# Performance work log

Measured on AMD Instinct MI355X. Metric: run time of the kernel, lower is better.

Reference implementation:

```python
import jax, jax.numpy as jnp
import numpy as np

B = 4096          # events
L = 524288        # total set points (avg 128 per event)
CIN = 16          # per-point feature size (set feature 'a')
DVEC = 32         # flat feature size (feature 'b')
PHI = [128, 128, 64]
MLP = [256, 128]
EPS = 1e-5        # BatchNorm1d eps


def setup_inputs() -> dict:
    key = jax.random.key(0)
    ks = jax.random.split(key, 10)
    def n(k, shape, scale=0.05):
        return jax.random.normal(k, shape, dtype=jnp.float32) * scale
    return {
        "x_a": jax.random.normal(ks[0], (1, CIN, L), dtype=jnp.float32),
        "x_b": jax.random.normal(ks[1], (B, DVEC), dtype=jnp.float32),
        # row 0 -> counts for set feature 'a'; row 1 ignored (Reshape branch)
        "sample_indices": jnp.full((2, B), L // B, dtype=jnp.int32),
        "W1": n(ks[2], (PHI[0], CIN)),  "b1": jnp.zeros((PHI[0],), jnp.float32),
        "W2": n(ks[3], (PHI[1], PHI[0])), "b2": jnp.zeros((PHI[1],), jnp.float32),
        "W3": n(ks[4], (PHI[2], PHI[1])), "b3": jnp.zeros((PHI[2],), jnp.float32),
        "Wm1": n(ks[5], (MLP[0], PHI[2] + DVEC)), "bm1": jnp.zeros((MLP[0],), jnp.float32),
        "g1": jnp.ones((MLP[0],), jnp.float32), "be1": jnp.zeros((MLP[0],), jnp.float32),
        "Wm2": n(ks[6], (MLP[1], MLP[0])), "bm2": jnp.zeros((MLP[1],), jnp.float32),
        "g2": jnp.ones((MLP[1],), jnp.float32), "be2": jnp.zeros((MLP[1],), jnp.float32),
        "Wm3": n(ks[7], (1, MLP[1])), "bm3": jnp.zeros((1,), jnp.float32),
    }


def _bn(x, g, b):
    # BatchNorm1d, training-mode batch stats, biased variance (torch semantics)
    mu = jnp.mean(x, axis=0)
    var = jnp.var(x, axis=0)
    return (x - mu) * jax.lax.rsqrt(var + EPS) * g + b


def reference(x_a, x_b, sample_indices,
              W1, b1, W2, b2, W3, b3,
              Wm1, bm1, g1, be1, Wm2, bm2, g2, be2, Wm3, bm3):
    counts = sample_indices[0].astype(jnp.int32)                       # [B]
    bounds = jnp.concatenate([jnp.zeros((1,), jnp.int32), jnp.cumsum(counts)])  # [B+1]

    # PhiNet: pointwise Conv1d stack (kernel size 1) on [CIN, L]
    h = x_a[0]
    h = jax.nn.relu(jnp.einsum('oc,cl->ol', W1, h) + b1[:, None])
    h = jax.nn.relu(jnp.einsum('oc,cl->ol', W2, h) + b2[:, None])
    h = jax.nn.relu(jnp.einsum('oc,cl->ol', W3, h) + b3[:, None])      # [64, L]

    # fused segment-mean: point p belongs to segment j iff bounds[j] <= p < bounds[j+1]
    seg = jnp.searchsorted(bounds, jnp.arange(h.shape[1], dtype=jnp.int32), side='right') - 1
    sums = jax.ops.segment_sum(h.T, seg, num_segments=counts.shape[0])  # [B, 64]
    means = sums / jnp.maximum(counts, 1).astype(jnp.float32)[:, None]

    # feature order: sorted keys -> ('a' set repr, 'b' flat)
    z = jnp.concatenate([means, x_b.reshape(-1, DVEC)], axis=1)        # [B, 96]

    z = jax.nn.relu(_bn(z @ Wm1.T + bm1, g1, be1))
    z = jax.nn.relu(_bn(z @ Wm2.T + bm2, g2, be2))
    return jax.nn.sigmoid(z @ Wm3.T + bm3)                             # [B, 1]
```

## Files before the change

### kernel.cpp

```cpp
#include <hip/hip_runtime.h>
#include <hip/hip_bf16.h>

#define B_EVENTS 4096
#define L_PTS    524288
#define CIN      16
#define C1       128
#define C2       128
#define C3       64
#define DVEC     32
#define ZDIM     96
#define M1       256
#define M2       128
#define BN_EPS   1e-5f
#define TILE     64
#define NTILES   (L_PTS / TILE)
#define GRID_PHI 2048
#define NTPB     (NTILES / GRID_PHI)

#define XOFF     0
#define H1OFF    4096
#define H2OFF    20480
#define LDSSZ    36864

typedef __attribute__((ext_vector_type(8))) short bf16x8;
typedef __attribute__((ext_vector_type(4))) float f32x4;

__device__ __forceinline__ unsigned cvtpk(float lo, float hi) {
    unsigned r;
    asm("v_cvt_pk_bf16_f32 %0, %1, %2" : "=v"(r) : "v"(lo), "v"(hi));
    return r;
}

__device__ __forceinline__ unsigned long long pack4relub(f32x4 a, f32x4 b) {
    union { unsigned u[2]; unsigned long long ll; } pk;
    pk.u[0] = cvtpk(fmaxf(a[0] + b[0], 0.f), fmaxf(a[1] + b[1], 0.f));
    pk.u[1] = cvtpk(fmaxf(a[2] + b[2], 0.f), fmaxf(a[3] + b[3], 0.f));
    return pk.ll;
}

__device__ __forceinline__ bf16x8 frag_from_f32(const float* p) {
    const float4 lo = *(const float4*)p;
    const float4 hi = *(const float4*)(p + 4);
    union { unsigned u[4]; bf16x8 v; } r;
    r.u[0] = cvtpk(lo.x, lo.y);
    r.u[1] = cvtpk(lo.z, lo.w);
    r.u[2] = cvtpk(hi.x, hi.y);
    r.u[3] = cvtpk(hi.z, hi.w);
    return r.v;
}

__device__ __forceinline__ int ldsoff(int base, int rowSlots, int c, int sir) {
    int s = c * rowSlots + sir;
    s ^= (c & 7);
    return base + s * 16;
}

__device__ __forceinline__ int xaddr(int pt, int g) {
    return XOFF + (((pt * 4 + g) ^ (pt & 7)) * 16);
}

__global__ __launch_bounds__(1024) void scan_kernel(const int* __restrict__ si,
                                                    int* __restrict__ bounds,
                                                    int* __restrict__ tilemap)
{
    __shared__ int sh[1024];
    const int tid = threadIdx.x;
    const int c0 = si[tid*4+0], c1 = si[tid*4+1], c2 = si[tid*4+2], c3 = si[tid*4+3];
    const int s4 = c0 + c1 + c2 + c3;
    sh[tid] = s4;
    __syncthreads();
    for (int off = 1; off < 1024; off <<= 1) {
        int add = (tid >= off) ? sh[tid - off] : 0;
        __syncthreads();
        sh[tid] += add;
        __syncthreads();
    }
    const int excl = (tid == 0) ? 0 : sh[tid - 1];
    bounds[tid*4+0] = excl;
    bounds[tid*4+1] = excl + c0;
    bounds[tid*4+2] = excl + c0 + c1;
    bounds[tid*4+3] = excl + c0 + c1 + c2;
    if (tid == 1023) bounds[B_EVENTS] = excl + s4;
    __syncthreads();

    const int total = bounds[B_EVENTS];
    for (int t = tid; t < NTILES; t += 1024) {
        const int p0 = t * TILE;
        if (p0 >= total) { tilemap[t] = -1; continue; }
        int e = (int)(((long long)p0 * B_EVENTS) / total);
        if (e > B_EVENTS - 1) e = B_EVENTS - 1;
        while (bounds[e] > p0) --e;
        while (bounds[e + 1] <= p0) ++e;
        const bool fast = (p0 + TILE <= bounds[e + 1]);
        tilemap[t] = e | (fast ? (1 << 30) : 0);
    }
}

__global__ __launch_bounds__(256, 3) void phi_mfma_kernel(
    const float* __restrict__ xa,
    const int* __restrict__ bounds, const int* __restrict__ tilemap,
    const float* __restrict__ W1, const float* __restrict__ W2, const float* __restrict__ W3,
    const float* __restrict__ b1, const float* __restrict__ b2, const float* __restrict__ b3,
    float* __restrict__ zsum)
{
    __shared__ __align__(16) char lds[LDSSZ];

    const int tid  = threadIdx.x;
    const int lane = tid & 63;
    const int wm   = tid >> 6;
    const int g4   = lane >> 4;
    const int c16  = lane & 15;

    const int pt = tid & 63;
    const int h  = tid >> 6;
    int t = blockIdx.x;
    float xv[4];
    #pragma unroll
    for (int jj = 0; jj < 4; ++jj)
        xv[jj] = xa[(size_t)(h * 4 + jj) * L_PTS + t * TILE + pt];

    f32x4 bb1[2], bb2[2], bb3;
    #pragma unroll
    for (int mf = 0; mf < 2; ++mf) {
        bb1[mf] = *(const f32x4*)&b1[wm * 32 + mf * 16 + g4 * 4];
        bb2[mf] = *(const f32x4*)&b2[wm * 32 + mf * 16 + g4 * 4];
    }
    bb3 = *(const f32x4*)&b3[wm * 16 + g4 * 4];

    bf16x8 a1[2], a2[2][4], a3[4];
    {
        const bf16x8 zz = {0, 0, 0, 0, 0, 0, 0, 0};
        const int r1 = wm * 32 + c16;
        #pragma unroll
        for (int mf = 0; mf < 2; ++mf)
            a1[mf] = (g4 < 2) ? frag_from_f32(&W1[(r1 + mf * 16) * CIN + g4 * 8]) : zz;
        #pragma unroll
        for (int mf = 0; mf < 2; ++mf)
            #pragma unroll
            for (int kf = 0; kf < 4; ++kf)
                a2[mf][kf] = frag_from_f32(&W2[(r1 + mf * 16) * C1 + kf * 32 + g4 * 8]);
        const int r3 = wm * 16 + c16;
        #pragma unroll
        for (int kf = 0; kf < 4; ++kf)
            a3[kf] = frag_from_f32(&W3[r3 * C2 + kf * 32 + g4 * 8]);
    }

    {
        const int zs = 2 + (h >> 1);
        *(unsigned long long*)(lds + (((pt * 4 + zs) ^ (pt & 7)) * 16) + (h & 1) * 8) = 0ull;
        union { unsigned u[2]; unsigned long long ll; } pk;
        pk.u[0] = cvtpk(xv[0], xv[1]);
        pk.u[1] = cvtpk(xv[2], xv[3]);
        *(unsigned long long*)(lds + xaddr(pt, h >> 1) + (h & 1) * 8) = pk.ll;
    }
    __syncthreads();

    for (int it = 0; it < NTPB; ++it) {
        const int tm = tilemap[t];
        if (tm < 0) break;
        const int  e0    = tm & 0x3FFFFFFF;
        const bool fastp = (tm >> 30) & 1;
        const int  p0    = t * TILE;
        const int  tn    = t + GRID_PHI;
        const bool more  = (it + 1 < NTPB);

        if (more) {
            #pragma unroll
            for (int jj = 0; jj < 4; ++jj)
                xv[jj] = xa[(size_t)(h * 4 + jj) * L_PTS + tn * TILE + pt];
        }

        {
            f32x4 acc[2][4];
            #pragma unroll
            for (int mf = 0; mf < 2; ++mf)
                #pragma unroll
                for (int nf = 0; nf < 4; ++nf)
                    acc[mf][nf] = f32x4{0.f, 0.f, 0.f, 0.f};
            bf16x8 bfr[4];
            #pragma unroll
            for (int nf = 0; nf < 4; ++nf)
                bfr[nf] = *(const bf16x8*)(lds + xaddr(nf * 16 + c16, g4));
            __builtin_amdgcn_s_setprio(1);
            #pragma unroll
            for (int nf = 0; nf < 4; ++nf)
                #pragma unroll
                for (int mf = 0; mf < 2; ++mf)
                    acc[mf][nf] = __builtin_amdgcn_mfma_f32_16x16x32_bf16(a1[mf], bfr[nf], acc[mf][nf], 0, 0, 0);
            __builtin_amdgcn_s_setprio(0);
            #pragma unroll
            for (int mf = 0; mf < 2; ++mf) {
                const int sir = wm * 4 + mf * 2 + (g4 >> 1);
                #pragma unroll
                for (int nf = 0; nf < 4; ++nf) {
                    const int c = nf * 16 + c16;
                    *(unsigned long long*)(lds + ldsoff(H1OFF, 16, c, sir) + (g4 & 1) * 8) = pack4relub(acc[mf][nf], bb1[mf]);
                }
            }
        }
        __syncthreads();

        {
            f32x4 acc[2][4];
            #pragma unroll
            for (int mf = 0; mf < 2; ++mf)
                #pragma unroll
                for (int nf = 0; nf < 4; ++nf)
                    acc[mf][nf] = f32x4{0.f, 0.f, 0.f, 0.f};
            #pragma unroll
            for (int nf = 0; nf < 4; ++nf) {
                const int c = nf * 16 + c16;
                bf16x8 bk[4];
                #pragma unroll
                for (int kf = 0; kf < 4; ++kf)
                    bk[kf] = *(const bf16x8*)(lds + ldsoff(H1OFF, 16, c, kf * 4 + g4));
                __builtin_amdgcn_s_setprio(1);
                #pragma unroll
                for (int mf = 0; mf < 2; ++mf)
                    #pragma unroll
                    for (int kf = 0; kf < 4; ++kf)
                        acc[mf][nf] = __builtin_amdgcn_mfma_f32_16x16x32_bf16(a2[mf][kf], bk[kf], acc[mf][nf], 0, 0, 0);
                __builtin_amdgcn_s_setprio(0);
            }
            if (more) {
                union { unsigned u[2]; unsigned long long ll; } pk;
                pk.u[0] = cvtpk(xv[0], xv[1]);
                pk.u[1] = cvtpk(xv[2], xv[3]);
                *(unsigned long long*)(lds + xaddr(pt, h >> 1) + (h & 1) * 8) = pk.ll;
            }
            #pragma unroll
            for (int mf = 0; mf < 2; ++mf) {
                const int sir = wm * 4 + mf * 2 + (g4 >> 1);
                #pragma unroll
                for (int nf = 0; nf < 4; ++nf) {
                    const int c = nf * 16 + c16;
                    *(unsigned long long*)(lds + ldsoff(H2OFF, 16, c, sir) + (g4 & 1) * 8) = pack4relub(acc[mf][nf], bb2[mf]);
                }
            }
        }
        __syncthreads();

        {
            f32x4 acc3[4];
            #pragma unroll
            for (int nf = 0; nf < 4; ++nf) acc3[nf] = f32x4{0.f, 0.f, 0.f, 0.f};
            #pragma unroll
            for (int nf = 0; nf < 4; ++nf) {
                const int c = nf * 16 + c16;
                bf16x8 bk[4];
                #pragma unroll
                for (int kf = 0; kf < 4; ++kf)
                    bk[kf] = *(const bf16x8*)(lds + ldsoff(H2OFF, 16, c, kf * 4 + g4));
                __builtin_amdgcn_s_setprio(1);
                #pragma unroll
                for (int kf = 0; kf < 4; ++kf)
                    acc3[nf] = __builtin_amdgcn_mfma_f32_16x16x32_bf16(a3[kf], bk[kf], acc3[nf], 0, 0, 0);
                __builtin_amdgcn_s_setprio(0);
            }

            if (fastp) {
                float s[4] = {0.f, 0.f, 0.f, 0.f};
                #pragma unroll
                for (int nf = 0; nf < 4; ++nf)
                    #pragma unroll
                    for (int r = 0; r < 4; ++r)
                        s[r] += fmaxf(acc3[nf][r] + bb3[r], 0.f);
                #pragma unroll
                for (int r = 0; r < 4; ++r) {
                    float v = s[r];
                    v += __shfl_xor(v, 1, 64);
                    v += __shfl_xor(v, 2, 64);
                    v += __shfl_xor(v, 4, 64);
                    v += __shfl_xor(v, 8, 64);
                    s[r] = v;
                }
                if (c16 == 0) {
                    #pragma unroll
                    for (int r = 0; r < 4; ++r)
                        atomicAdd(&zsum[(size_t)e0 * C3 + wm * 16 + g4 * 4 + r], s[r]);
                }
            } else {
                const int total = bounds[B_EVENTS];
                #pragma unroll
                for (int nf = 0; nf < 4; ++nf) {
                    const int col = p0 + nf * 16 + c16;
                    if (col < total) {
                        int sgr = e0;
                        while (col >= bounds[sgr + 1]) ++sgr;
                        #pragma unroll
                        for (int r = 0; r < 4; ++r)
                            atomicAdd(&zsum[(size_t)sgr * C3 + wm * 16 + g4 * 4 + r],
                                      fmaxf(acc3[nf][r] + bb3[r], 0.f));
                    }
                }
            }
        }
        t = tn;
    }
}

__global__ __launch_bounds__(256) void mlp1_kernel(
    const float* __restrict__ zsum, const int* __restrict__ si, const float* __restrict__ xb,
    const float* __restrict__ Wm1, const float* __restrict__ bm1,
    float* __restrict__ y1, float* __restrict__ gsum, float* __restrict__ gsq)
{
    __shared__ float zs[8][ZDIM + 4];
    const int r0 = blockIdx.x * 8;
    const int tid = threadIdx.x;
    for (int i = tid; i < 8 * ZDIM; i += 256) {
        const int r = i / ZDIM, c = i - r * ZDIM;
        float v;
        if (c < C3) {
            const int cnt = si[r0 + r];
            v = zsum[(size_t)(r0 + r) * C3 + c] / (float)max(cnt, 1);
        } else {
            v = xb[(size_t)(r0 + r) * DVEC + (c - C3)];
        }
        zs[r][c] = v;
    }
    __syncthreads();
    const int o = tid;
    float acc[8];
    const float bb = bm1[o];
    #pragma unroll
    for (int r = 0; r < 8; ++r) acc[r] = bb;
    for (int c = 0; c < ZDIM; c += 4) {
        const float4 w = *(const float4*)&Wm1[o * ZDIM + c];
        #pragma unroll
        for (int r = 0; r < 8; ++r) {
            const float4 v = *(const float4*)&zs[r][c];
            acc[r] += w.x*v.x + w.y*v.y + w.z*v.z + w.w*v.w;
        }
    }
    float s = 0.f, sq = 0.f;
    #pragma unroll
    for (int r = 0; r < 8; ++r) {
        y1[(size_t)(r0 + r) * M1 + o] = acc[r];
        s += acc[r]; sq += acc[r] * acc[r];
    }
    atomicAdd(&gsum[o], s);
    atomicAdd(&gsq[o], sq);
}

__global__ __launch_bounds__(256) void mlp2_kernel(
    const float* __restrict__ y1,
    const float* __restrict__ gsum1, const float* __restrict__ gsq1,
    const float* __restrict__ g1, const float* __restrict__ be1,
    const float* __restrict__ Wm2, const float* __restrict__ bm2,
    float* __restrict__ y2, float* __restrict__ gsum, float* __restrict__ gsq)
{
    __shared__ float zs[8][M1 + 4];
    __shared__ float sc[M1], sh[M1];
    const int r0 = blockIdx.x * 8;
    const int tid = threadIdx.x;
    {
        const float mu  = gsum1[tid] * (1.f / B_EVENTS);
        const float var = gsq1[tid] * (1.f / B_EVENTS) - mu * mu;
        const float s0  = rsqrtf(var + BN_EPS) * g1[tid];
        sc[tid] = s0;
        sh[tid] = be1[tid] - mu * s0;
    }
    __syncthreads();
    for (int i = tid; i < 8 * M1; i += 256) {
        const int r = i >> 8, c = i & (M1 - 1);
        const float v = y1[(size_t)(r0 + r) * M1 + c];
        zs[r][c] = fmaxf(v * sc[c] + sh[c], 0.f);
    }
    __syncthreads();
    const int o = tid & 127;
    const int h = tid >> 7;
    float acc[4];
    const float bb = bm2[o];
    #pragma unroll
    for (int r = 0; r < 4; ++r) acc[r] = bb;
    for (int c = 0; c < M1; c += 4) {
        const float4 w = *(const float4*)&Wm2[o * M1 + c];
        #pragma unroll
        for (int r = 0; r < 4; ++r) {
            const float4 v = *(const float4*)&zs[h * 4 + r][c];
            acc[r] += w.x*v.x + w.y*v.y + w.z*v.z + w.w*v.w;
        }
    }
    float s = 0.f, sq = 0.f;
    #pragma unroll
    for (int r = 0; r < 4; ++r) {
        y2[(size_t)(r0 + h * 4 + r) * M2 + o] = acc[r];
        s += acc[r]; sq += acc[r] * acc[r];
    }
    atomicAdd(&gsum[o], s);
    atomicAdd(&gsq[o], sq);
}

__global__ __launch_bounds__(256) void final_kernel(
    const float* __restrict__ y2,
    const float* __restrict__ gsum2, const float* __restrict__ gsq2,
    const float* __restrict__ g2, const float* __restrict__ be2,
    const float* __restrict__ Wm3, const float* __restrict__ bm3,
    float* __restrict__ out)
{
    __shared__ float sc[M2], sh[M2];
    const int tid = threadIdx.x;
    if (tid < M2) {
        const float mu  = gsum2[tid] * (1.f / B_EVENTS);
        const float var = gsq2[tid] * (1.f / B_EVENTS) - mu * mu;
        const float s0  = rsqrtf(var + BN_EPS) * g2[tid];
        sc[tid] = s0;
        sh[tid] = be2[tid] - mu * s0;
    }
    __syncthreads();
    const int w = tid >> 6, l = tid & 63;
    const int r = blockIdx.x * 4 + w;
    const float e0 = fmaxf(y2[(size_t)r * M2 + l]      * sc[l]      + sh[l],      0.f);
    const float e1 = fmaxf(y2[(size_t)r * M2 + 64 + l] * sc[64 + l] + sh[64 + l], 0.f);
    float a = e0 * Wm3[l] + e1 * Wm3[64 + l];
    #pragma unroll
    for (int off = 32; off >= 1; off >>= 1) a += __shfl_down(a, off, 64);
    if (l == 0) out[r] = 1.f / (1.f + expf(-(a + bm3[0])));
}

extern "C" void kernel_launch(void* const* d_in, const int* in_sizes, int n_in,
                              void* d_out, int out_size, void* d_ws, size_t ws_size,
                              hipStream_t stream) {
    const float* xa  = (const float*)d_in[0];
    const float* xb  = (const float*)d_in[1];
    const int*   si  = (const int*)  d_in[2];
    const float* W1  = (const float*)d_in[3];
    const float* b1  = (const float*)d_in[4];
    const float* W2  = (const float*)d_in[5];
    const float* b2  = (const float*)d_in[6];
    const float* W3  = (const float*)d_in[7];
    const float* b3  = (const float*)d_in[8];
    const float* Wm1 = (const float*)d_in[9];
    const float* bm1 = (const float*)d_in[10];
    const float* g1  = (const float*)d_in[11];
    const float* be1 = (const float*)d_in[12];
    const float* Wm2 = (const float*)d_in[13];
    const float* bm2 = (const float*)d_in[14];
    const float* g2  = (const float*)d_in[15];
    const float* be2 = (const float*)d_in[16];
    const float* Wm3 = (const float*)d_in[17];
    const float* bm3 = (const float*)d_in[18];
    float* out = (float*)d_out;

    char* ws = (char*)d_ws;
    size_t off = 0;
    auto alloc = [&](size_t bytes) -> void* {
        void* p = ws + off;
        off = (off + bytes + 255) & ~(size_t)255;
        return p;
    };
    float* zsum    = (float*)alloc((size_t)B_EVENTS * C3 * sizeof(float));
    float* stats   = (float*)alloc(768 * sizeof(float));
    int*   bounds  = (int*)  alloc((B_EVENTS + 1) * sizeof(int));
    int*   tilemap = (int*)  alloc(NTILES * sizeof(int));
    float* y1      = (float*)alloc((size_t)B_EVENTS * M1 * sizeof(float));
    float* y2      = (float*)alloc((size_t)B_EVENTS * M2 * sizeof(float));
    float* gsum1 = stats;
    float* gsq1  = stats + 256;
    float* gsum2 = stats + 512;
    float* gsq2  = stats + 640;

    hipMemsetAsync(zsum, 0, (size_t)B_EVENTS * C3 * sizeof(float) + 768 * sizeof(float), stream);

    hipLaunchKernelGGL(scan_kernel, dim3(1), dim3(1024), 0, stream, si, bounds, tilemap);
    hipLaunchKernelGGL(phi_mfma_kernel, dim3(GRID_PHI), dim3(256), 0, stream,
                       xa, bounds, tilemap, W1, W2, W3, b1, b2, b3, zsum);
    hipLaunchKernelGGL(mlp1_kernel, dim3(B_EVENTS / 8), dim3(256), 0, stream,
                       zsum, si, xb, Wm1, bm1, y1, gsum1, gsq1);
    hipLaunchKernelGGL(mlp2_kernel, dim3(B_EVENTS / 8), dim3(256), 0, stream,
                       y1, gsum1, gsq1, g1, be1, Wm2, bm2, y2, gsum2, gsq2);
    hipLaunchKernelGGL(final_kernel, dim3(B_EVENTS / 4), dim3(256), 0, stream,
                       y2, gsum2, gsq2, g2, be2, Wm3, bm3, out);
}
```

Measured before the change: 137.6 us.

## Retile phi MFMA waves as 2x2 M/N grid, bias in LDS, fold memset into scan

The phi kernel's four waves are rearranged from a 4x1 split over output channels into a 2x2 split over channels and points. Each wave now covers 64 channels by 32 points, so every LDS B-fragment load feeds more MFMAs, at the cost of holding twice as many weight fragments in registers. Biases move from registers into LDS to offset that register growth. The separate hipMemsetAsync is replaced by a second block of the scan kernel that zeroes the accumulators, which removes one launch.

```diff
diff --git a/kernel.cpp b/kernel.cpp
--- a/kernel.cpp
+++ b/kernel.cpp
@@ -20,7 +20,10 @@
 #define XOFF     0
 #define H1OFF    4096
 #define H2OFF    20480
-#define LDSSZ    36864
+#define BIAS1    36864
+#define BIAS2    37376
+#define BIAS3    37888
+#define LDSSZ    38144
 
 typedef __attribute__((ext_vector_type(8))) short bf16x8;
 typedef __attribute__((ext_vector_type(4))) float f32x4;
@@ -61,10 +64,15 @@
 
 __global__ __launch_bounds__(1024) void scan_kernel(const int* __restrict__ si,
                                                     int* __restrict__ bounds,
-                                                    int* __restrict__ tilemap)
+                                                    int* __restrict__ tilemap,
+                                                    float* __restrict__ zsum)
 {
+    const int tid = threadIdx.x;
+    if (blockIdx.x == 1) {
+        for (int i = tid; i < B_EVENTS * C3 + 768; i += 1024) zsum[i] = 0.f;
+        return;
+    }
     __shared__ int sh[1024];
-    const int tid = threadIdx.x;
     const int c0 = si[tid*4+0], c1 = si[tid*4+1], c2 = si[tid*4+2], c3 = si[tid*4+3];
     const int s4 = c0 + c1 + c2 + c3;
     sh[tid] = s4;
@@ -107,7 +115,9 @@
 
     const int tid  = threadIdx.x;
     const int lane = tid & 63;
-    const int wm   = tid >> 6;
+    const int wid  = tid >> 6;
+    const int wm   = wid >> 1;
+    const int wn   = wid & 1;
     const int g4   = lane >> 4;
     const int c16  = lane & 15;
 
@@ -119,30 +129,31 @@
     for (int jj = 0; jj < 4; ++jj)
         xv[jj] = xa[(size_t)(h * 4 + jj) * L_PTS + t * TILE + pt];
 
-    f32x4 bb1[2], bb2[2], bb3;
-    #pragma unroll
-    for (int mf = 0; mf < 2; ++mf) {
-        bb1[mf] = *(const f32x4*)&b1[wm * 32 + mf * 16 + g4 * 4];
-        bb2[mf] = *(const f32x4*)&b2[wm * 32 + mf * 16 + g4 * 4];
-    }
-    bb3 = *(const f32x4*)&b3[wm * 16 + g4 * 4];
-
-    bf16x8 a1[2], a2[2][4], a3[4];
+    if (tid < 128) {
+        ((float*)(lds + BIAS1))[tid] = b1[tid];
+        ((float*)(lds + BIAS2))[tid] = b2[tid];
+    } else if (tid < 192) {
+        ((float*)(lds + BIAS3))[tid - 128] = b3[tid - 128];
+    }
+
+    bf16x8 a1[4], a2[4][4], a3[2][4];
     {
         const bf16x8 zz = {0, 0, 0, 0, 0, 0, 0, 0};
-        const int r1 = wm * 32 + c16;
-        #pragma unroll
-        for (int mf = 0; mf < 2; ++mf)
+        const int r1 = wm * 64 + c16;
+        #pragma unroll
+        for (int mf = 0; mf < 4; ++mf)
             a1[mf] = (g4 < 2) ? frag_from_f32(&W1[(r1 + mf * 16) * CIN + g4 * 8]) : zz;
         #pragma unroll
-        for (int mf = 0; mf < 2; ++mf)
+        for (int mf = 0; mf < 4; ++mf)
             #pragma unroll
             for (int kf = 0; kf < 4; ++kf)
                 a2[mf][kf] = frag_from_f32(&W2[(r1 + mf * 16) * C1 + kf * 32 + g4 * 8]);
-        const int r3 = wm * 16 + c16;
-        #pragma unroll
-        for (int kf = 0; kf < 4; ++kf)
-            a3[kf] = frag_from_f32(&W3[r3 * C2 + kf * 32 + g4 * 8]);
+        const int r3 = wm * 32 + c16;
+        #pragma unroll
+        for (int mf = 0; mf < 2; ++mf)
+            #pragma unroll
+            for (int kf = 0; kf < 4; ++kf)
+                a3[mf][kf] = frag_from_f32(&W3[(r3 + mf * 16) * C2 + kf * 32 + g4 * 8]);
     }
 
     {
@@ -170,128 +181,128 @@
                 xv[jj] = xa[(size_t)(h * 4 + jj) * L_PTS + tn * TILE + pt];
         }
 
-        {
-            f32x4 acc[2][4];
-            #pragma unroll
-            for (int mf = 0; mf < 2; ++mf)
-                #pragma unroll
-                for (int nf = 0; nf < 4; ++nf)
-                    acc[mf][nf] = f32x4{0.f, 0.f, 0.f, 0.f};
-            bf16x8 bfr[4];
-            #pragma unroll
-            for (int nf = 0; nf < 4; ++nf)
-                bfr[nf] = *(const bf16x8*)(lds + xaddr(nf * 16 + c16, g4));
+        #pragma unroll
+        for (int nf = 0; nf < 2; ++nf) {
+            const int c = wn * 32 + nf * 16 + c16;
+            f32x4 acc[4];
+            #pragma unroll
+            for (int mf = 0; mf < 4; ++mf) acc[mf] = f32x4{0.f, 0.f, 0.f, 0.f};
+            const bf16x8 bfr = *(const bf16x8*)(lds + xaddr(c, g4));
             __builtin_amdgcn_s_setprio(1);
             #pragma unroll
-            for (int nf = 0; nf < 4; ++nf)
-                #pragma unroll
-                for (int mf = 0; mf < 2; ++mf)
-                    acc[mf][nf] = __builtin_amdgcn_mfma_f32_16x16x32_bf16(a1[mf], bfr[nf], acc[mf][nf], 0, 0, 0);
+            for (int mf = 0; mf < 4; ++mf)
+                acc[mf] = __builtin_amdgcn_mfma_f32_16x16x32_bf16(a1[mf], bfr, acc[mf], 0, 0, 0);
             __builtin_amdgcn_s_setprio(0);
             #pragma unroll
-            for (int mf = 0; mf < 2; ++mf) {
-                const int sir = wm * 4 + mf * 2 + (g4 >> 1);
-                #pragma unroll
-                for (int nf = 0; nf < 4; ++nf) {
-                    const int c = nf * 16 + c16;
-                    *(unsigned long long*)(lds + ldsoff(H1OFF, 16, c, sir) + (g4 & 1) * 8) = pack4relub(acc[mf][nf], bb1[mf]);
-                }
+            for (int mf = 0; mf < 4; ++mf) {
+                const f32x4 bb = *(const f32x4*)(lds + BIAS1 + (wm * 64 + mf * 16 + g4 * 4) * 4);
+                const int sir = wm * 8 + mf * 2 + (g4 >> 1);
+                *(unsigned long long*)(lds + ldsoff(H1OFF, 16, c, sir) + (g4 & 1) * 8) = pack4relub(acc[mf], bb);
             }
         }
         __syncthreads();
 
-        {
-            f32x4 acc[2][4];
-            #pragma unroll
-            for (int mf = 0; mf < 2; ++mf)
-                #pragma unroll
-                for (int nf = 0; nf < 4; ++nf)
-                    acc[mf][nf] = f32x4{0.f, 0.f, 0.f, 0.f};
-            #pragma unroll
-            for (int nf = 0; nf < 4; ++nf) {
-                const int c = nf * 16 + c16;
-                bf16x8 bk[4];
+        #pragma unroll
+        for (int nf = 0; nf < 2; ++nf) {
+            const int c = wn * 32 + nf * 16 + c16;
+            f32x4 acc[4];
+            #pragma unroll
+            for (int mf = 0; mf < 4; ++mf) acc[mf] = f32x4{0.f, 0.f, 0.f, 0.f};
+            bf16x8 bk[4];
+            #pragma unroll
+            for (int kf = 0; kf < 4; ++kf)
+                bk[kf] = *(const bf16x8*)(lds + ldsoff(H1OFF, 16, c, kf * 4 + g4));
+            __builtin_amdgcn_s_setprio(1);
+            #pragma unroll
+            for (int mf = 0; mf < 4; ++mf)
                 #pragma unroll
                 for (int kf = 0; kf < 4; ++kf)
-                    bk[kf] = *(const bf16x8*)(lds + ldsoff(H1OFF, 16, c, kf * 4 + g4));
-                __builtin_amdgcn_s_setprio(1);
-                #pragma unroll
-                for (int mf = 0; mf < 2; ++mf)
-                    #pragma unroll
-                    for (int kf = 0; kf < 4; ++kf)
-                        acc[mf][nf] = __builtin_amdgcn_mfma_f32_16x16x32_bf16(a2[mf][kf], bk[kf], acc[mf][nf], 0, 0, 0);
-                __builtin_amdgcn_s_setprio(0);
-            }
-            if (more) {
+                    acc[mf] = __builtin_amdgcn_mfma_f32_16x16x32_bf16(a2[mf][kf], bk[kf], acc[mf], 0, 0, 0);
+            __builtin_amdgcn_s_setprio(0);
+            if (nf == 0 && more) {
                 union { unsigned u[2]; unsigned long long ll; } pk;
                 pk.u[0] = cvtpk(xv[0], xv[1]);
                 pk.u[1] = cvtpk(xv[2], xv[3]);
                 *(unsigned long long*)(lds + xaddr(pt, h >> 1) + (h & 1) * 8) = pk.ll;
             }
             #pragma unroll
-            for (int mf = 0; mf < 2; ++mf) {
-                const int sir = wm * 4 + mf * 2 + (g4 >> 1);
+            for (int mf = 0; mf < 4; ++mf) {
+                const f32x4 bb = *(const f32x4*)(lds + BIAS2 + (wm * 64 + mf * 16 + g4 * 4) * 4);
+                const int sir = wm * 8 + mf * 2 + (g4 >> 1);
+                *(unsigned long long*)(lds + ldsoff(H2OFF, 16, c, sir) + (g4 & 1) * 8) = pack4relub(acc[mf], bb);
+            }
+        }
+        __syncthreads();
+
+        {
+            float s[2][4];
+            #pragma unroll
+            for (int mf = 0; mf < 2; ++mf)
                 #pragma unroll
-                for (int nf = 0; nf < 4; ++nf) {
-                    const int c = nf * 16 + c16;
-                    *(unsigned long long*)(lds + ldsoff(H2OFF, 16, c, sir) + (g4 & 1) * 8) = pack4relub(acc[mf][nf], bb2[mf]);
-                }
-            }
-        }
-        __syncthreads();
-
-        {
-            f32x4 acc3[4];
-            #pragma unroll
-            for (int nf = 0; nf < 4; ++nf) acc3[nf] = f32x4{0.f, 0.f, 0.f, 0.f};
-            #pragma unroll
-            for (int nf = 0; nf < 4; ++nf) {
-                const int c = nf * 16 + c16;
+                for (int r = 0; r < 4; ++r) s[mf][r] = 0.f;
+
+            #pragma unroll
+            for (int nf = 0; nf < 2; ++nf) {
+                const int c = wn * 32 + nf * 16 + c16;
+                f32x4 acc3[2];
+                acc3[0] = f32x4{0.f, 0.f, 0.f, 0.f};
+                acc3[1] = f32x4{0.f, 0.f, 0.f, 0.f};
                 bf16x8 bk[4];
                 #pragma unroll
                 for (int kf = 0; kf < 4; ++kf)
                     bk[kf] = *(const bf16x8*)(lds + ldsoff(H2OFF, 16, c, kf * 4 + g4));
                 __builtin_amdgcn_s_setprio(1);
                 #pragma unroll
-                for (int kf = 0; kf < 4; ++kf)
-                    acc3[nf] = __builtin_amdgcn_mfma_f32_16x16x32_bf16(a3[kf], bk[kf], acc3[nf], 0, 0, 0);
+                for (int mf = 0; mf < 2; ++mf)
+                    #pragma unroll
+                    for (int kf = 0; kf < 4; ++kf)
+                        acc3[mf] = __builtin_amdgcn_mfma_f32_16x16x32_bf16(a3[mf][kf], bk[kf], acc3[mf], 0, 0, 0);
                 __builtin_amdgcn_s_setprio(0);
-            }
-
-            if (fastp) {
-                float s[4] = {0.f, 0.f, 0.f, 0.f};
-                #pragma unroll
-                for (int nf = 0; nf < 4; ++nf)
+
+                if (fastp) {
                     #pragma unroll
-                    for (int r = 0; r < 4; ++r)
-                        s[r] += fmaxf(acc3[nf][r] + bb3[r], 0.f);
-                #pragma unroll
-                for (int r = 0; r < 4; ++r) {
-                    float v = s[r];
-                    v += __shfl_xor(v, 1, 64);
-                    v += __shfl_xor(v, 2, 64);
-                    v += __shfl_xor(v, 4, 64);
-                    v += __shfl_xor(v, 8, 64);
-                    s[r] = v;
-                }
-                if (c16 == 0) {
-                    #pragma unroll
-                    for (int r = 0; r < 4; ++r)
-                        atomicAdd(&zsum[(size_t)e0 * C3 + wm * 16 + g4 * 4 + r], s[r]);
-                }
-            } else {
-                const int total = bounds[B_EVENTS];
-                #pragma unroll
-                for (int nf = 0; nf < 4; ++nf) {
-                    const int col = p0 + nf * 16 + c16;
+                    for (int mf = 0; mf < 2; ++mf) {
+                        const f32x4 bb = *(const f32x4*)(lds + BIAS3 + (wm * 32 + mf * 16 + g4 * 4) * 4);
+                        #pragma unroll
+                        for (int r = 0; r < 4; ++r)
+                            s[mf][r] += fmaxf(acc3[mf][r] + bb[r], 0.f);
+                    }
+                } else {
+                    const int total = bounds[B_EVENTS];
+                    const int col = p0 + c;
                     if (col < total) {
                         int sgr = e0;
                         while (col >= bounds[sgr + 1]) ++sgr;
                         #pragma unroll
+                        for (int mf = 0; mf < 2; ++mf) {
+                            const f32x4 bb = *(const f32x4*)(lds + BIAS3 + (wm * 32 + mf * 16 + g4 * 4) * 4);
+                            #pragma unroll
+                            for (int r = 0; r < 4; ++r)
+                                atomicAdd(&zsum[(size_t)sgr * C3 + wm * 32 + mf * 16 + g4 * 4 + r],
+                                          fmaxf(acc3[mf][r] + bb[r], 0.f));
+                        }
+                    }
+                }
+            }
+
+            if (fastp) {
+                #pragma unroll
+                for (int mf = 0; mf < 2; ++mf)
+                    #pragma unroll
+                    for (int r = 0; r < 4; ++r) {
+                        float v = s[mf][r];
+                        v += __shfl_xor(v, 1, 64);
+                        v += __shfl_xor(v, 2, 64);
+                        v += __shfl_xor(v, 4, 64);
+                        v += __shfl_xor(v, 8, 64);
+                        s[mf][r] = v;
+                    }
+                if (c16 == 0) {
+                    #pragma unroll
+                    for (int mf = 0; mf < 2; ++mf)
+                        #pragma unroll
                         for (int r = 0; r < 4; ++r)
-                            atomicAdd(&zsum[(size_t)sgr * C3 + wm * 16 + g4 * 4 + r],
-                                      fmaxf(acc3[nf][r] + bb3[r], 0.f));
-                    }
+                            atomicAdd(&zsum[(size_t)e0 * C3 + wm * 32 + mf * 16 + g4 * 4 + r], s[mf][r]);
                 }
             }
         }
@@ -460,9 +471,7 @@
     float* gsum2 = stats + 512;
     float* gsq2  = stats + 640;
 
-    hipMemsetAsync(zsum, 0, (size_t)B_EVENTS * C3 * sizeof(float) + 768 * sizeof(float), stream);
-
-    hipLaunchKernelGGL(scan_kernel, dim3(1), dim3(1024), 0, stream, si, bounds, tilemap);
+    hipLaunchKernelGGL(scan_kernel, dim3(2), dim3(1024), 0, stream, si, bounds, tilemap, zsum);
     hipLaunchKernelGGL(phi_mfma_kernel, dim3(GRID_PHI), dim3(256), 0, stream,
                        xa, bounds, tilemap, W1, W2, W3, b1, b2, b3, zsum);
     hipLaunchKernelGGL(mlp1_kernel, dim3(B_EVENTS / 8), dim3(256), 0, stream,
```

New measurement: 182.3 us. 1.33x slower.

## Halve phi tile to 32 points, raise occupancy, fold zsum memset into scan

Applied to the files above, without the earlier changes.

Shrinks the per-iteration point tile from 64 to 32, which halves LDS use and the accumulator register footprint, and raises launch bounds to 4 blocks per CU. Only half the threads now load input features, while the rest zero the padding slots. Separately, the zsum/stats memset is replaced by a second block of the scan kernel, removing one runtime memset call. In exchange, each tile feeds fewer MFMAs per barrier, there are twice as many loop iterations and barriers, and each 32-point tile issues its own atomic adds on the fast path, roughly doubling atomic traffic.

```diff
diff --git a/kernel.cpp b/kernel.cpp
--- a/kernel.cpp
+++ b/kernel.cpp
@@ -12,15 +12,15 @@
 #define M1       256
 #define M2       128
 #define BN_EPS   1e-5f
-#define TILE     64
+#define TILE     32
 #define NTILES   (L_PTS / TILE)
 #define GRID_PHI 2048
 #define NTPB     (NTILES / GRID_PHI)
 
 #define XOFF     0
-#define H1OFF    4096
-#define H2OFF    20480
-#define LDSSZ    36864
+#define H1OFF    2048
+#define H2OFF    10240
+#define LDSSZ    18432
 
 typedef __attribute__((ext_vector_type(8))) short bf16x8;
 typedef __attribute__((ext_vector_type(4))) float f32x4;
@@ -61,10 +61,15 @@
 
 __global__ __launch_bounds__(1024) void scan_kernel(const int* __restrict__ si,
                                                     int* __restrict__ bounds,
-                                                    int* __restrict__ tilemap)
+                                                    int* __restrict__ tilemap,
+                                                    float* __restrict__ zsum)
 {
+    const int tid = threadIdx.x;
+    if (blockIdx.x == 1) {
+        for (int i = tid; i < B_EVENTS * C3 + 768; i += 1024) zsum[i] = 0.f;
+        return;
+    }
     __shared__ int sh[1024];
-    const int tid = threadIdx.x;
     const int c0 = si[tid*4+0], c1 = si[tid*4+1], c2 = si[tid*4+2], c3 = si[tid*4+3];
     const int s4 = c0 + c1 + c2 + c3;
     sh[tid] = s4;
@@ -96,7 +101,7 @@
     }
 }
 
-__global__ __launch_bounds__(256, 3) void phi_mfma_kernel(
+__global__ __launch_bounds__(256, 4) void phi_mfma_kernel(
     const float* __restrict__ xa,
     const int* __restrict__ bounds, const int* __restrict__ tilemap,
     const float* __restrict__ W1, const float* __restrict__ W2, const float* __restrict__ W3,
@@ -111,13 +116,15 @@
     const int g4   = lane >> 4;
     const int c16  = lane & 15;
 
-    const int pt = tid & 63;
-    const int h  = tid >> 6;
+    const int pt = tid & 31;
+    const int q  = tid >> 5;
     int t = blockIdx.x;
     float xv[4];
-    #pragma unroll
-    for (int jj = 0; jj < 4; ++jj)
-        xv[jj] = xa[(size_t)(h * 4 + jj) * L_PTS + t * TILE + pt];
+    if (q < 4) {
+        #pragma unroll
+        for (int jj = 0; jj < 4; ++jj)
+            xv[jj] = xa[(size_t)(q * 4 + jj) * L_PTS + t * TILE + pt];
+    }
 
     f32x4 bb1[2], bb2[2], bb3;
     #pragma unroll
@@ -145,13 +152,14 @@
             a3[kf] = frag_from_f32(&W3[r3 * C2 + kf * 32 + g4 * 8]);
     }
 
-    {
-        const int zs = 2 + (h >> 1);
-        *(unsigned long long*)(lds + (((pt * 4 + zs) ^ (pt & 7)) * 16) + (h & 1) * 8) = 0ull;
+    if (q >= 4) {
+        const int zs = 2 + ((q - 4) >> 1);
+        *(unsigned long long*)(lds + xaddr(pt, zs) + (q & 1) * 8) = 0ull;
+    } else {
         union { unsigned u[2]; unsigned long long ll; } pk;
         pk.u[0] = cvtpk(xv[0], xv[1]);
         pk.u[1] = cvtpk(xv[2], xv[3]);
-        *(unsigned long long*)(lds + xaddr(pt, h >> 1) + (h & 1) * 8) = pk.ll;
+        *(unsigned long long*)(lds + xaddr(pt, q >> 1) + (q & 1) * 8) = pk.ll;
     }
     __syncthreads();
 
@@ -164,26 +172,26 @@
         const int  tn    = t + GRID_PHI;
         const bool more  = (it + 1 < NTPB);
 
-        if (more) {
+        if (more && q < 4) {
             #pragma unroll
             for (int jj = 0; jj < 4; ++jj)
-                xv[jj] = xa[(size_t)(h * 4 + jj) * L_PTS + tn * TILE + pt];
+                xv[jj] = xa[(size_t)(q * 4 + jj) * L_PTS + tn * TILE + pt];
         }
 
         {
-            f32x4 acc[2][4];
-            #pragma unroll
-            for (int mf = 0; mf < 2; ++mf)
-                #pragma unroll
-                for (int nf = 0; nf < 4; ++nf)
-                    acc[mf][nf] = f32x4{0.f, 0.f, 0.f, 0.f};
-            bf16x8 bfr[4];
-            #pragma unroll
-            for (int nf = 0; nf < 4; ++nf)
+            f32x4 acc[2][2];
+            #pragma unroll
+            for (int mf = 0; mf < 2; ++mf) {
+                acc[mf][0] = f32x4{0.f, 0.f, 0.f, 0.f};
+                acc[mf][1] = f32x4{0.f, 0.f, 0.f, 0.f};
+            }
+            bf16x8 bfr[2];
+            #pragma unroll
+            for (int nf = 0; nf < 2; ++nf)
                 bfr[nf] = *(const bf16x8*)(lds + xaddr(nf * 16 + c16, g4));
             __builtin_amdgcn_s_setprio(1);
             #pragma unroll
-            for (int nf = 0; nf < 4; ++nf)
+            for (int nf = 0; nf < 2; ++nf)
                 #pragma unroll
                 for (int mf = 0; mf < 2; ++mf)
                     acc[mf][nf] = __builtin_amdgcn_mfma_f32_16x16x32_bf16(a1[mf], bfr[nf], acc[mf][nf], 0, 0, 0);
@@ -192,7 +200,7 @@
             for (int mf = 0; mf < 2; ++mf) {
                 const int sir = wm * 4 + mf * 2 + (g4 >> 1);
                 #pragma unroll
-                for (int nf = 0; nf < 4; ++nf) {
+                for (int nf = 0; nf < 2; ++nf) {
                     const int c = nf * 16 + c16;
                     *(unsigned long long*)(lds + ldsoff(H1OFF, 16, c, sir) + (g4 & 1) * 8) = pack4relub(acc[mf][nf], bb1[mf]);
                 }
@@ -201,14 +209,14 @@
         __syncthreads();
 
         {
-            f32x4 acc[2][4];
-            #pragma unroll
-            for (int mf = 0; mf < 2; ++mf)
-                #pragma unroll
-                for (int nf = 0; nf < 4; ++nf)
-                    acc[mf][nf] = f32x4{0.f, 0.f, 0.f, 0.f};
-            #pragma unroll
-            for (int nf = 0; nf < 4; ++nf) {
+            f32x4 acc[2][2];
+            #pragma unroll
+            for (int mf = 0; mf < 2; ++mf) {
+                acc[mf][0] = f32x4{0.f, 0.f, 0.f, 0.f};
+                acc[mf][1] = f32x4{0.f, 0.f, 0.f, 0.f};
+            }
+            #pragma unroll
+            for (int nf = 0; nf < 2; ++nf) {
                 const int c = nf * 16 + c16;
                 bf16x8 bk[4];
                 #pragma unroll
@@ -222,17 +230,17 @@
                         acc[mf][nf] = __builtin_amdgcn_mfma_f32_16x16x32_bf16(a2[mf][kf], bk[kf], acc[mf][nf], 0, 0, 0);
                 __builtin_amdgcn_s_setprio(0);
             }
-            if (more) {
+            if (more && q < 4) {
                 union { unsigned u[2]; unsigned long long ll; } pk;
                 pk.u[0] = cvtpk(xv[0], xv[1]);
                 pk.u[1] = cvtpk(xv[2], xv[3]);
-                *(unsigned long long*)(lds + xaddr(pt, h >> 1) + (h & 1) * 8) = pk.ll;
+                *(unsigned long long*)(lds + xaddr(pt, q >> 1) + (q & 1) * 8) = pk.ll;
             }
             #pragma unroll
             for (int mf = 0; mf < 2; ++mf) {
                 const int sir = wm * 4 + mf * 2 + (g4 >> 1);
                 #pragma unroll
-                for (int nf = 0; nf < 4; ++nf) {
+                for (int nf = 0; nf < 2; ++nf) {
                     const int c = nf * 16 + c16;
                     *(unsigned long long*)(lds + ldsoff(H2OFF, 16, c, sir) + (g4 & 1) * 8) = pack4relub(acc[mf][nf], bb2[mf]);
                 }
@@ -241,11 +249,11 @@
         __syncthreads();
 
         {
-            f32x4 acc3[4];
-            #pragma unroll
-            for (int nf = 0; nf < 4; ++nf) acc3[nf] = f32x4{0.f, 0.f, 0.f, 0.f};
-            #pragma unroll
-            for (int nf = 0; nf < 4; ++nf) {
+            f32x4 acc3[2];
+            acc3[0] = f32x4{0.f, 0.f, 0.f, 0.f};
+            acc3[1] = f32x4{0.f, 0.f, 0.f, 0.f};
+            #pragma unroll
+            for (int nf = 0; nf < 2; ++nf) {
                 const int c = nf * 16 + c16;
                 bf16x8 bk[4];
                 #pragma unroll
@@ -259,12 +267,11 @@
             }
 
             if (fastp) {
-                float s[4] = {0.f, 0.f, 0.f, 0.f};
-                #pragma unroll
-                for (int nf = 0; nf < 4; ++nf)
-                    #pragma unroll
-                    for (int r = 0; r < 4; ++r)
-                        s[r] += fmaxf(acc3[nf][r] + bb3[r], 0.f);
+                float s[4];
+                #pragma unroll
+                for (int r = 0; r < 4; ++r)
+                    s[r] = fmaxf(acc3[0][r] + bb3[r], 0.f)
+                         + fmaxf(acc3[1][r] + bb3[r], 0.f);
                 #pragma unroll
                 for (int r = 0; r < 4; ++r) {
                     float v = s[r];
@@ -282,7 +289,7 @@
             } else {
                 const int total = bounds[B_EVENTS];
                 #pragma unroll
-                for (int nf = 0; nf < 4; ++nf) {
+                for (int nf = 0; nf < 2; ++nf) {
                     const int col = p0 + nf * 16 + c16;
                     if (col < total) {
                         int sgr = e0;
@@ -460,9 +467,7 @@
     float* gsum2 = stats + 512;
     float* gsq2  = stats + 640;
 
-    hipMemsetAsync(zsum, 0, (size_t)B_EVENTS * C3 * sizeof(float) + 768 * sizeof(float), stream);
-
-    hipLaunchKernelGGL(scan_kernel, dim3(1), dim3(1024), 0, stream, si, bounds, tilemap);
+    hipLaunchKernelGGL(scan_kernel, dim3(2), dim3(1024), 0, stream, si, bounds, tilemap, zsum);
     hipLaunchKernelGGL(phi_mfma_kernel, dim3(GRID_PHI), dim3(256), 0, stream,
                        xa, bounds, tilemap, W1, W2, W3, b1, b2, b3, zsum);
     hipLaunchKernelGGL(mlp1_kernel, dim3(B_EVENTS / 8), dim3(256), 0, stream,
```

After: 139.9 us. No clear change (+1.7%).
